# Kernel optimization log

Hardware: AMD Instinct MI355X
Metric: run time of the kernel (lower is better)

## Reference

```python
import jax, jax.numpy as jnp
import numpy as np

DIM = 256
HEADS = 8
WIN = (2, 7, 7)
BW = 512
NW = 64  # num windows (mask leading dim); BW % NW == 0


def _relative_position_index(win):
    Wz, Wh, Ww = win
    coords = np.stack(np.meshgrid(np.arange(Wz), np.arange(Wh), np.arange(Ww), indexing='ij'))
    cf = coords.reshape(3, -1)  # (3, N)
    rel = cf[:, :, None] - cf[:, None, :]  # (3, N, N)
    rel = rel.transpose(1, 2, 0).copy()
    rel[:, :, 0] += Wz - 1
    rel[:, :, 1] += Wh - 1
    rel[:, :, 2] += Ww - 1
    rel[:, :, 0] *= (2 * Wh - 1) * (2 * Ww - 1)
    rel[:, :, 1] *= 2 * Ww - 1
    return rel.sum(-1).astype(np.int32)  # (N, N)


def setup_inputs() -> dict:
    key = jax.random.key(0)
    ks = jax.random.split(key, 8)
    N = WIN[0] * WIN[1] * WIN[2]
    table_size = (2 * WIN[0] - 1) * (2 * WIN[1] - 1) * (2 * WIN[2] - 1)
    return {
        'x': jax.random.normal(ks[0], (BW, N, DIM), dtype=jnp.float32),
        'qkv_w': jax.random.normal(ks[1], (DIM, 3 * DIM), dtype=jnp.float32) * 0.02,
        'qkv_b': jax.random.normal(ks[2], (3 * DIM,), dtype=jnp.float32) * 0.02,
        'bias_table': jax.random.normal(ks[3], (table_size, HEADS), dtype=jnp.float32) * 0.02,
        'proj_w': jax.random.normal(ks[4], (DIM, DIM), dtype=jnp.float32) * 0.02,
        'proj_b': jax.random.normal(ks[5], (DIM,), dtype=jnp.float32) * 0.02,
        'mask': jax.random.normal(ks[6], (NW, N, N), dtype=jnp.float32),
        'rpi': jnp.asarray(_relative_position_index(WIN)),
    }


def reference(x, qkv_w, qkv_b, bias_table, proj_w, proj_b, mask, rpi):
    BW_, N, C = x.shape
    H = HEADS
    D = C // H
    scale = D ** (-0.5)
    # qkv projection -> (3, BW, H, N, D)
    qkv = (x @ qkv_w + qkv_b).reshape(BW_, N, 3, H, D).transpose(2, 0, 3, 1, 4)
    q, k, v = qkv[0], qkv[1], qkv[2]
    attn = jnp.einsum('bhnd,bhmd->bhnm', q * scale, k)  # (BW, H, N, N)
    # relative position bias gather: (N, N, H) -> (H, N, N)
    bias = bias_table[rpi.reshape(-1)].reshape(N, N, H).transpose(2, 0, 1)
    attn = attn + bias[None]
    nW = mask.shape[0]
    attn = attn.reshape(BW_ // nW, nW, H, N, N) + mask[None, :, None]
    attn = attn.reshape(BW_, H, N, N)
    attn = jax.nn.softmax(attn, axis=-1)
    out = jnp.einsum('bhnm,bhmd->bhnd', attn, v)
    out = out.transpose(0, 2, 1, 3).reshape(BW_, N, C)
    return out @ proj_w + proj_b
```

## Files before the change

kernel.cpp:

```cpp
#include <hip/hip_runtime.h>
#include <math.h>

typedef short bf8v __attribute__((ext_vector_type(8)));
typedef float f32x4 __attribute__((ext_vector_type(4)));

#define SCALE 0.17677669529663687f

__device__ __forceinline__ unsigned short f2bf(float f) {
    union { float f; unsigned int u; } c; c.f = f;
    unsigned int r = (c.u + 0x7FFFu + ((c.u >> 16) & 1u)) >> 16;
    return (unsigned short)r;
}

__device__ __forceinline__ int sw32(int row, int k8) {
    return row * 32 + ((k8 ^ ((row >> 1) & 3)) << 3);
}
__device__ __forceinline__ int sw128(int row, int c8) {
    return row * 128 + (((c8 ^ row) & 15) << 3);
}

__global__ __launch_bounds__(256) void cvt_x_kernel(const float* __restrict__ in,
                                                    unsigned short* __restrict__ out, int n8) {
    int i = blockIdx.x * 256 + threadIdx.x;
    if (i >= n8) return;
    const float4* p = (const float4*)(in + (size_t)i * 8);
    float4 a = p[0], b = p[1];
    union { int4 v; unsigned short u[8]; } o;
    o.u[0]=f2bf(a.x); o.u[1]=f2bf(a.y); o.u[2]=f2bf(a.z); o.u[3]=f2bf(a.w);
    o.u[4]=f2bf(b.x); o.u[5]=f2bf(b.y); o.u[6]=f2bf(b.z); o.u[7]=f2bf(b.w);
    *(int4*)(out + (size_t)i * 8) = o.v;
}

__global__ __launch_bounds__(256) void tcvt_w_kernel(const float* __restrict__ in,
                                                     unsigned short* __restrict__ out, int C) {
    int idx = blockIdx.x * 256 + threadIdx.x;
    int c = idx >> 8, r = idx & 255;
    if (c < C) out[idx] = f2bf(in[r * C + c]);
}

__global__ __launch_bounds__(256) void bm_kernel(const float* __restrict__ bias_table,
                                                 const int* __restrict__ rpi,
                                                 const float* __restrict__ mask,
                                                 float* __restrict__ bm) {
    int bx = blockIdx.x;
    int w = bx >> 3, h = bx & 7;
    const float* mp = mask + (size_t)w * 9604;
    float* op = bm + (size_t)bx * 9604;
    for (int e = threadIdx.x; e < 9604; e += 256)
        op[e] = bias_table[rpi[e] * 8 + h] + mp[e];
}

__global__ __launch_bounds__(256) void qkv_gemm_kernel(
    const unsigned short* __restrict__ A, const unsigned short* __restrict__ B,
    const float* __restrict__ bias,
    unsigned short* __restrict__ q, unsigned short* __restrict__ k, unsigned short* __restrict__ v)
{
    __shared__ unsigned short As[128 * 32];
    __shared__ unsigned short Bs[128 * 32];
    const int tid = threadIdx.x;
    const int lane = tid & 63, wid = tid >> 6;
    const int l16 = lane & 15, lg = lane >> 4;
    const int wr = wid >> 1, wc = wid & 1;
    const int bm0 = blockIdx.y * 128, bn0 = blockIdx.x * 128;

    f32x4 acc[4][4] = {};
    const int crow = tid >> 2, ck8 = tid & 3;

    for (int k0 = 0; k0 < 256; k0 += 32) {
        __syncthreads();
        *(int4*)&As[sw32(crow,      ck8)] = *(const int4*)(A + (size_t)(bm0 + crow     ) * 256 + k0 + ck8 * 8);
        *(int4*)&As[sw32(crow + 64, ck8)] = *(const int4*)(A + (size_t)(bm0 + crow + 64) * 256 + k0 + ck8 * 8);
        *(int4*)&Bs[sw32(crow,      ck8)] = *(const int4*)(B + (size_t)(bn0 + crow     ) * 256 + k0 + ck8 * 8);
        *(int4*)&Bs[sw32(crow + 64, ck8)] = *(const int4*)(B + (size_t)(bn0 + crow + 64) * 256 + k0 + ck8 * 8);
        __syncthreads();
        bf8v af[4], bfr[4];
        #pragma unroll
        for (int mt = 0; mt < 4; ++mt) af[mt]  = *(const bf8v*)&As[sw32(wr*64 + mt*16 + l16, lg)];
        #pragma unroll
        for (int nt = 0; nt < 4; ++nt) bfr[nt] = *(const bf8v*)&Bs[sw32(wc*64 + nt*16 + l16, lg)];
        #pragma unroll
        for (int mt = 0; mt < 4; ++mt)
            #pragma unroll
            for (int nt = 0; nt < 4; ++nt)
                acc[mt][nt] = __builtin_amdgcn_mfma_f32_16x16x32_bf16(af[mt], bfr[nt], acc[mt][nt], 0, 0, 0);
    }

    #pragma unroll
    for (int mt = 0; mt < 4; ++mt) {
        #pragma unroll
        for (int r = 0; r < 4; ++r) {
            const int row = bm0 + wr*64 + mt*16 + lg*4 + r;
            const int bi = row / 98, n = row - bi * 98;
            const size_t rb = ((size_t)bi * 8 * 98 + n) * 32;
            #pragma unroll
            for (int nt = 0; nt < 4; ++nt) {
                const int col = bn0 + wc*64 + nt*16 + l16;
                const float val = acc[mt][nt][r] + bias[col];
                const int h = (col >> 5) & 7, d = col & 31;
                const size_t o = rb + (size_t)h * (98 * 32) + d;
                if (col < 256)      q[o] = f2bf(val * SCALE);
                else if (col < 512) k[o] = f2bf(val);
                else                v[o] = f2bf(val);
            }
        }
    }
}

__global__ __launch_bounds__(448) void attn_kernel(
    const unsigned short* __restrict__ q, const unsigned short* __restrict__ k,
    const unsigned short* __restrict__ v, const float* __restrict__ bm,
    unsigned short* __restrict__ att)
{
    __shared__ unsigned short Qs[112 * 32];
    __shared__ unsigned short Ks[112 * 32];
    __shared__ unsigned short Vt[32 * 128];
    __shared__ unsigned short Ps[112 * 128];

    const int bh = blockIdx.x;
    const int b = bh >> 3, h = bh & 7;
    const int tid = threadIdx.x;
    const int wid = tid >> 6, lane = tid & 63;
    const int l16 = lane & 15, lg = lane >> 4;
    const unsigned short* qp = q + (size_t)bh * 3136;
    const unsigned short* kp = k + (size_t)bh * 3136;
    const unsigned short* vp = v + (size_t)bh * 3136;

    if (tid < 392) {
        const int row = tid >> 2, k8 = tid & 3;
        *(int4*)&Qs[sw32(row, k8)] = *(const int4*)(qp + row * 32 + k8 * 8);
        *(int4*)&Ks[sw32(row, k8)] = *(const int4*)(kp + row * 32 + k8 * 8);
        union { int4 v; unsigned short u[8]; } t;
        t.v = *(const int4*)(vp + row * 32 + k8 * 8);
        #pragma unroll
        for (int j = 0; j < 8; ++j) {
            const int d = k8 * 8 + j;
            Vt[sw128(d, row >> 3) + (row & 7)] = t.u[j];
        }
    } else {
        const int t2 = tid - 392;
        const int row = 98 + (t2 >> 2), k8 = t2 & 3;
        const int4 z = {0, 0, 0, 0};
        *(int4*)&Qs[sw32(row, k8)] = z;
        *(int4*)&Ks[sw32(row, k8)] = z;
    }
    for (int e = tid; e < 32 * 30; e += 448) {
        const int d = e / 30, n = 98 + e - (e / 30) * 30;
        Vt[sw128(d, n >> 3) + (n & 7)] = 0;
    }
    __syncthreads();

    const int rt = wid;
    const bf8v qf = *(const bf8v*)&Qs[sw32(rt * 16 + l16, lg)];
    f32x4 sa[7];
    const f32x4 zero = {0.f, 0.f, 0.f, 0.f};
    #pragma unroll
    for (int ct = 0; ct < 7; ++ct) {
        const bf8v kf = *(const bf8v*)&Ks[sw32(ct * 16 + l16, lg)];
        sa[ct] = __builtin_amdgcn_mfma_f32_16x16x32_bf16(qf, kf, zero, 0, 0, 0);
    }

    const float* bmp = bm + (size_t)((b & 63) * 8 + h) * 9604;
    #pragma unroll
    for (int ct = 0; ct < 7; ++ct) {
        const int col = ct * 16 + l16;
        const int colc = col < 98 ? col : 97;
        #pragma unroll
        for (int r = 0; r < 4; ++r) {
            const int row = rt * 16 + lg * 4 + r;
            const int rowc = row < 98 ? row : 97;
            const float add = bmp[rowc * 98 + colc];
            sa[ct][r] = (col < 98) ? (sa[ct][r] + add) : -INFINITY;
        }
    }

    #pragma unroll
    for (int r = 0; r < 4; ++r) {
        float mx = sa[0][r];
        #pragma unroll
        for (int ct = 1; ct < 7; ++ct) mx = fmaxf(mx, sa[ct][r]);
        #pragma unroll
        for (int off = 1; off < 16; off <<= 1) mx = fmaxf(mx, __shfl_xor(mx, off));
        float sum = 0.f;
        #pragma unroll
        for (int ct = 0; ct < 7; ++ct) { const float e = __expf(sa[ct][r] - mx); sa[ct][r] = e; sum += e; }
        #pragma unroll
        for (int off = 1; off < 16; off <<= 1) sum += __shfl_xor(sum, off);
        const float inv = 1.0f / sum;
        const int row = rt * 16 + lg * 4 + r;
        #pragma unroll
        for (int ct = 0; ct < 7; ++ct) {
            const int col = ct * 16 + l16;
            Ps[sw128(row, col >> 3) + (col & 7)] = f2bf(sa[ct][r] * inv);
        }
    }
    #pragma unroll
    for (int e0 = 0; e0 < 4; ++e0) {
        const int e = e0 * 64 + lane;
        const int row = rt * 16 + (e >> 4), col = 112 + (e & 15);
        Ps[sw128(row, col >> 3) + (col & 7)] = 0;
    }

    f32x4 oacc[2] = {};
    #pragma unroll
    for (int ks = 0; ks < 4; ++ks) {
        const bf8v pf = *(const bf8v*)&Ps[sw128(rt * 16 + l16, ks * 4 + lg)];
        #pragma unroll
        for (int dt = 0; dt < 2; ++dt) {
            const bf8v vf = *(const bf8v*)&Vt[sw128(dt * 16 + l16, ks * 4 + lg)];
            oacc[dt] = __builtin_amdgcn_mfma_f32_16x16x32_bf16(pf, vf, oacc[dt], 0, 0, 0);
        }
    }

    #pragma unroll
    for (int r = 0; r < 4; ++r) {
        const int row = rt * 16 + lg * 4 + r;
        if (row < 98) {
            #pragma unroll
            for (int dt = 0; dt < 2; ++dt)
                att[((size_t)b * 98 + row) * 256 + h * 32 + dt * 16 + l16] = f2bf(oacc[dt][r]);
        }
    }
}

__global__ __launch_bounds__(256) void proj_gemm_kernel(
    const unsigned short* __restrict__ A, const unsigned short* __restrict__ B,
    const float* __restrict__ pb, float* __restrict__ out)
{
    __shared__ unsigned short As[128 * 32];
    __shared__ unsigned short Bs[128 * 32];
    const int tid = threadIdx.x;
    const int lane = tid & 63, wid = tid >> 6;
    const int l16 = lane & 15, lg = lane >> 4;
    const int wr = wid >> 1, wc = wid & 1;
    const int bm0 = blockIdx.y * 128, bn0 = blockIdx.x * 128;

    f32x4 acc[4][4] = {};
    const int crow = tid >> 2, ck8 = tid & 3;

    for (int k0 = 0; k0 < 256; k0 += 32) {
        __syncthreads();
        *(int4*)&As[sw32(crow,      ck8)] = *(const int4*)(A + (size_t)(bm0 + crow     ) * 256 + k0 + ck8 * 8);
        *(int4*)&As[sw32(crow + 64, ck8)] = *(const int4*)(A + (size_t)(bm0 + crow + 64) * 256 + k0 + ck8 * 8);
        *(int4*)&Bs[sw32(crow,      ck8)] = *(const int4*)(B + (size_t)(bn0 + crow     ) * 256 + k0 + ck8 * 8);
        *(int4*)&Bs[sw32(crow + 64, ck8)] = *(const int4*)(B + (size_t)(bn0 + crow + 64) * 256 + k0 + ck8 * 8);
        __syncthreads();
        bf8v af[4], bfr[4];
        #pragma unroll
        for (int mt = 0; mt < 4; ++mt) af[mt]  = *(const bf8v*)&As[sw32(wr*64 + mt*16 + l16, lg)];
        #pragma unroll
        for (int nt = 0; nt < 4; ++nt) bfr[nt] = *(const bf8v*)&Bs[sw32(wc*64 + nt*16 + l16, lg)];
        #pragma unroll
        for (int mt = 0; mt < 4; ++mt)
            #pragma unroll
            for (int nt = 0; nt < 4; ++nt)
                acc[mt][nt] = __builtin_amdgcn_mfma_f32_16x16x32_bf16(af[mt], bfr[nt], acc[mt][nt], 0, 0, 0);
    }

    #pragma unroll
    for (int mt = 0; mt < 4; ++mt)
        #pragma unroll
        for (int r = 0; r < 4; ++r) {
            const int row = bm0 + wr*64 + mt*16 + lg*4 + r;
            #pragma unroll
            for (int nt = 0; nt < 4; ++nt) {
                const int col = bn0 + wc*64 + nt*16 + l16;
                out[(size_t)row * 256 + col] = acc[mt][nt][r] + pb[col];
            }
        }
}

extern "C" void kernel_launch(void* const* d_in, const int* in_sizes, int n_in,
                              void* d_out, int out_size, void* d_ws, size_t ws_size,
                              hipStream_t stream) {
    const float* x          = (const float*)d_in[0];
    const float* qkv_w      = (const float*)d_in[1];
    const float* qkv_b      = (const float*)d_in[2];
    const float* bias_table = (const float*)d_in[3];
    const float* proj_w     = (const float*)d_in[4];
    const float* proj_b     = (const float*)d_in[5];
    const float* mask       = (const float*)d_in[6];
    const int*   rpi        = (const int*)d_in[7];
    float* out = (float*)d_out;

    const size_t SEG = (size_t)50176 * 256;
    unsigned short* xb  = (unsigned short*)d_ws;
    unsigned short* wtq = xb + SEG;
    unsigned short* wtp = wtq + 768 * 256;
    unsigned short* qb  = wtp + 256 * 256;
    unsigned short* kb  = qb + SEG;
    unsigned short* vb  = kb + SEG;
    unsigned short* attb = vb + SEG;
    float* bm = (float*)(attb + SEG);

    cvt_x_kernel<<<6272, 256, 0, stream>>>(x, xb, (int)(SEG / 8));
    tcvt_w_kernel<<<768, 256, 0, stream>>>(qkv_w, wtq, 768);
    tcvt_w_kernel<<<256, 256, 0, stream>>>(proj_w, wtp, 256);
    bm_kernel<<<512, 256, 0, stream>>>(bias_table, rpi, mask, bm);

    qkv_gemm_kernel<<<dim3(6, 392), 256, 0, stream>>>(xb, wtq, qkv_b, qb, kb, vb);
    attn_kernel<<<4096, 448, 0, stream>>>(qb, kb, vb, bm, attb);
    proj_gemm_kernel<<<dim3(2, 392), 256, 0, stream>>>(attb, wtp, proj_b, out);
}
```

Baseline: 265.7 us.

## Stage QKV epilogue through LDS, store row-major qkv, remap block order

```diff
diff --git a/kernel.cpp b/kernel.cpp
--- a/kernel.cpp
+++ b/kernel.cpp
@@ -17,6 +17,9 @@
 }
 __device__ __forceinline__ int sw128(int row, int c8) {
     return row * 128 + (((c8 ^ row) & 15) << 3);
+}
+__device__ __forceinline__ int bidx(int row, int col) {
+    return row * 128 + ((((col >> 3) ^ (((row >> 2) & 3) << 1)) & 15) << 3) + (col & 7);
 }
 
 __global__ __launch_bounds__(256) void cvt_x_kernel(const float* __restrict__ in,
@@ -52,16 +55,17 @@
 
 __global__ __launch_bounds__(256) void qkv_gemm_kernel(
     const unsigned short* __restrict__ A, const unsigned short* __restrict__ B,
-    const float* __restrict__ bias,
-    unsigned short* __restrict__ q, unsigned short* __restrict__ k, unsigned short* __restrict__ v)
+    const float* __restrict__ bias, unsigned short* __restrict__ qkv)
 {
     __shared__ unsigned short As[128 * 32];
     __shared__ unsigned short Bs[128 * 32];
+    __shared__ unsigned short Cb[128 * 128];
     const int tid = threadIdx.x;
     const int lane = tid & 63, wid = tid >> 6;
     const int l16 = lane & 15, lg = lane >> 4;
     const int wr = wid >> 1, wc = wid & 1;
-    const int bm0 = blockIdx.y * 128, bn0 = blockIdx.x * 128;
+    const int nb = (blockIdx.x & 7) * 294 + (blockIdx.x >> 3);
+    const int bm0 = (nb / 6) * 128, bn0 = (nb % 6) * 128;
 
     f32x4 acc[4][4] = {};
     const int crow = tid >> 2, ck8 = tid & 3;
@@ -86,29 +90,30 @@
     }
 
     #pragma unroll
-    for (int mt = 0; mt < 4; ++mt) {
-        #pragma unroll
-        for (int r = 0; r < 4; ++r) {
-            const int row = bm0 + wr*64 + mt*16 + lg*4 + r;
-            const int bi = row / 98, n = row - bi * 98;
-            const size_t rb = ((size_t)bi * 8 * 98 + n) * 32;
-            #pragma unroll
-            for (int nt = 0; nt < 4; ++nt) {
-                const int col = bn0 + wc*64 + nt*16 + l16;
-                const float val = acc[mt][nt][r] + bias[col];
-                const int h = (col >> 5) & 7, d = col & 31;
-                const size_t o = rb + (size_t)h * (98 * 32) + d;
-                if (col < 256)      q[o] = f2bf(val * SCALE);
-                else if (col < 512) k[o] = f2bf(val);
-                else                v[o] = f2bf(val);
+    for (int nt = 0; nt < 4; ++nt) {
+        const int colg = bn0 + wc * 64 + nt * 16 + l16;
+        const float bv = bias[colg];
+        const float sc = (colg < 256) ? SCALE : 1.0f;
+        #pragma unroll
+        for (int mt = 0; mt < 4; ++mt)
+            #pragma unroll
+            for (int r = 0; r < 4; ++r) {
+                const int rl = wr * 64 + mt * 16 + lg * 4 + r;
+                Cb[bidx(rl, wc * 64 + nt * 16 + l16)] = f2bf((acc[mt][nt][r] + bv) * sc);
             }
-        }
+    }
+    __syncthreads();
+    #pragma unroll
+    for (int c0 = 0; c0 < 8; ++c0) {
+        const int c = c0 * 256 + tid;
+        const int row = c >> 4, c8 = c & 15;
+        const int4 val = *(const int4*)&Cb[row * 128 + (((c8 ^ (((row >> 2) & 3) << 1)) & 15) << 3)];
+        *(int4*)(qkv + (size_t)(bm0 + row) * 768 + bn0 + c8 * 8) = val;
     }
 }
 
 __global__ __launch_bounds__(448) void attn_kernel(
-    const unsigned short* __restrict__ q, const unsigned short* __restrict__ k,
-    const unsigned short* __restrict__ v, const float* __restrict__ bm,
+    const unsigned short* __restrict__ qkv, const float* __restrict__ bm,
     unsigned short* __restrict__ att)
 {
     __shared__ unsigned short Qs[112 * 32];
@@ -116,21 +121,20 @@
     __shared__ unsigned short Vt[32 * 128];
     __shared__ unsigned short Ps[112 * 128];
 
-    const int bh = blockIdx.x;
-    const int b = bh >> 3, h = bh & 7;
+    const int nb = (blockIdx.x & 7) * 512 + (blockIdx.x >> 3);
+    const int b = nb >> 3, h = nb & 7;
     const int tid = threadIdx.x;
     const int wid = tid >> 6, lane = tid & 63;
     const int l16 = lane & 15, lg = lane >> 4;
-    const unsigned short* qp = q + (size_t)bh * 3136;
-    const unsigned short* kp = k + (size_t)bh * 3136;
-    const unsigned short* vp = v + (size_t)bh * 3136;
+    const unsigned short* base = qkv + (size_t)b * 98 * 768 + h * 32;
 
     if (tid < 392) {
         const int row = tid >> 2, k8 = tid & 3;
-        *(int4*)&Qs[sw32(row, k8)] = *(const int4*)(qp + row * 32 + k8 * 8);
-        *(int4*)&Ks[sw32(row, k8)] = *(const int4*)(kp + row * 32 + k8 * 8);
+        const unsigned short* rp = base + (size_t)row * 768 + k8 * 8;
+        *(int4*)&Qs[sw32(row, k8)] = *(const int4*)(rp);
+        *(int4*)&Ks[sw32(row, k8)] = *(const int4*)(rp + 256);
         union { int4 v; unsigned short u[8]; } t;
-        t.v = *(const int4*)(vp + row * 32 + k8 * 8);
+        t.v = *(const int4*)(rp + 512);
         #pragma unroll
         for (int j = 0; j < 8; ++j) {
             const int d = k8 * 8 + j;
@@ -232,7 +236,8 @@
     const int lane = tid & 63, wid = tid >> 6;
     const int l16 = lane & 15, lg = lane >> 4;
     const int wr = wid >> 1, wc = wid & 1;
-    const int bm0 = blockIdx.y * 128, bn0 = blockIdx.x * 128;
+    const int nb = (blockIdx.x & 7) * 98 + (blockIdx.x >> 3);
+    const int bm0 = (nb >> 1) * 128, bn0 = (nb & 1) * 128;
 
     f32x4 acc[4][4] = {};
     const int crow = tid >> 2, ck8 = tid & 3;
@@ -283,13 +288,11 @@
     float* out = (float*)d_out;
 
     const size_t SEG = (size_t)50176 * 256;
-    unsigned short* xb  = (unsigned short*)d_ws;
-    unsigned short* wtq = xb + SEG;
-    unsigned short* wtp = wtq + 768 * 256;
-    unsigned short* qb  = wtp + 256 * 256;
-    unsigned short* kb  = qb + SEG;
-    unsigned short* vb  = kb + SEG;
-    unsigned short* attb = vb + SEG;
+    unsigned short* xb   = (unsigned short*)d_ws;
+    unsigned short* wtq  = xb + SEG;
+    unsigned short* wtp  = wtq + 768 * 256;
+    unsigned short* qkvb = wtp + 256 * 256;
+    unsigned short* attb = qkvb + 3 * SEG;
     float* bm = (float*)(attb + SEG);
 
     cvt_x_kernel<<<6272, 256, 0, stream>>>(x, xb, (int)(SEG / 8));
@@ -297,7 +300,7 @@
     tcvt_w_kernel<<<256, 256, 0, stream>>>(proj_w, wtp, 256);
     bm_kernel<<<512, 256, 0, stream>>>(bias_table, rpi, mask, bm);
 
-    qkv_gemm_kernel<<<dim3(6, 392), 256, 0, stream>>>(xb, wtq, qkv_b, qb, kb, vb);
-    attn_kernel<<<4096, 448, 0, stream>>>(qb, kb, vb, bm, attb);
-    proj_gemm_kernel<<<dim3(2, 392), 256, 0, stream>>>(attb, wtp, proj_b, out);
-}
+    qkv_gemm_kernel<<<2352, 256, 0, stream>>>(xb, wtq, qkv_b, qkvb);
+    attn_kernel<<<4096, 448, 0, stream>>>(qkvb, bm, attb);
+    proj_gemm_kernel<<<784, 256, 0, stream>>>(attb, wtp, proj_b, out);
+}
```

Result: no change. 262.8 us (-1.1%).
